# Kernel optimization log

Measured on AMD Instinct MI355X. Metric: run time of the kernel, lower is better.

Reference implementation:

```python
import jax, jax.numpy as jnp
import numpy as np

NEG_INF = -100000000.0  # matches masked_fill value in torch source

def setup_inputs() -> dict:
    key = jax.random.key(0)
    ks = jax.random.split(key, 7)
    d_model, d = 1024, 128
    B, S = 4, 2048
    scale = 1.0 / np.sqrt(d_model)
    x = jax.random.normal(ks[0], (B, S, d_model), dtype=jnp.float32)
    Wq = jax.random.normal(ks[1], (d, d_model), dtype=jnp.float32) * scale
    bq = jax.random.normal(ks[2], (d,), dtype=jnp.float32) * 0.02
    Wk = jax.random.normal(ks[3], (d, d_model), dtype=jnp.float32) * scale
    bk = jax.random.normal(ks[4], (d,), dtype=jnp.float32) * 0.02
    Wv = jax.random.normal(ks[5], (d, d_model), dtype=jnp.float32) * scale
    bv = jax.random.normal(ks[6], (d,), dtype=jnp.float32) * 0.02
    return {"x": x, "Wq": Wq, "bq": bq, "Wk": Wk, "bk": bk, "Wv": Wv, "bv": bv}

def reference(x, Wq, bq, Wk, bk, Wv, bv):
    # Q,K,V: [B,S,d] via torch Linear (x @ W.T + b)
    Q = jnp.einsum('bsm,dm->bsd', x, Wq) + bq
    K = jnp.einsum('bsm,dm->bsd', x, Wk) + bk
    V = jnp.einsum('bsm,dm->bsd', x, Wv) + bv
    d = Wk.shape[0]
    scale = 1.0 / jnp.sqrt(jnp.asarray(d, dtype=Q.dtype))
    scores = jnp.einsum('bqd,bkd->bqk', Q, K) * scale  # [B,S,S]
    # Faithful to source: tril then value-based mask (tril==0 -> -1e8).
    tril = jnp.tril(scores)
    masked = jnp.where(tril == 0, NEG_INF, tril)
    attn = jax.nn.softmax(masked, axis=-1)
    context = jnp.einsum('bqk,bkd->bqd', attn, V)
    return context
```

## Files before the change

### kernel.cpp

```cpp
#include <hip/hip_runtime.h>

typedef __attribute__((ext_vector_type(8))) short bf16x8;
typedef __attribute__((ext_vector_type(4))) float f32x4;

__device__ __forceinline__ unsigned short f2bf(float f) {
    unsigned int u = __float_as_uint(f);
    u += 0x7fffu + ((u >> 16) & 1u);
    return (unsigned short)(u >> 16);
}
__device__ __forceinline__ unsigned int pack2bf(float lo, float hi) {
    return (unsigned int)f2bf(lo) | ((unsigned int)f2bf(hi) << 16);
}
__device__ __forceinline__ void async_ld16(void* lds, const void* g) {
    __builtin_amdgcn_global_load_lds(
        (const __attribute__((address_space(1))) unsigned int*)g,
        (__attribute__((address_space(3))) unsigned int*)lds, 16, 0, 0);
}

__global__ __launch_bounds__(256) void convert_bf16(
    const float* __restrict__ x,
    const float* __restrict__ Wq, const float* __restrict__ Wk,
    const float* __restrict__ Wv,
    unsigned short* __restrict__ xbf, unsigned short* __restrict__ Wcat)
{
    const size_t XN8 = (size_t)8192 * 1024 / 8;
    const size_t TN8 = XN8 + (size_t)3 * 128 * 1024 / 8;
    size_t i = (size_t)blockIdx.x * blockDim.x + threadIdx.x;
    const size_t stride = (size_t)gridDim.x * blockDim.x;
    for (; i < TN8; i += stride) {
        const float* src;
        unsigned short* dst;
        if (i < XN8) {
            src = x + i * 8;
            dst = xbf + i * 8;
        } else {
            size_t o = (i - XN8) * 8;
            int sel = (int)(o >> 17);
            const float* W = (sel == 0) ? Wq : ((sel == 1) ? Wk : Wv);
            src = W + (o & 131071);
            dst = Wcat + o;
        }
        float4 f0 = ((const float4*)src)[0];
        float4 f1 = ((const float4*)src)[1];
        uint4 u;
        u.x = pack2bf(f0.x, f0.y); u.y = pack2bf(f0.z, f0.w);
        u.z = pack2bf(f1.x, f1.y); u.w = pack2bf(f1.z, f1.w);
        *(uint4*)dst = u;
    }
}

__global__ __launch_bounds__(256) void qkv_gemm(
    const unsigned short* __restrict__ xbf,
    const unsigned short* __restrict__ Wcat,
    const float* __restrict__ bq, const float* __restrict__ bk,
    const float* __restrict__ bv,
    unsigned short* __restrict__ Qg,
    unsigned short* __restrict__ Kg,
    unsigned short* __restrict__ Vtg)
{
    __shared__ unsigned short As[64 * 64];
    __shared__ unsigned short Bs[128 * 64];

    const int tid  = threadIdx.x;
    const int lane = tid & 63;
    const int w    = tid >> 6;
    const int quad = lane >> 4;
    const int ln   = lane & 15;
    const int wm   = w >> 1, wn = w & 1;
    const int lr   = lane >> 3;
    const int lc   = (lane & 7) * 8;

    const int bid   = blockIdx.x;
    const int mbase = (bid / 3) * 64;
    const int nb    = bid % 3;
    const unsigned short* Wsel = Wcat + (size_t)nb * 128 * 1024;

    f32x4 acc[2][4];
#pragma unroll
    for (int mt = 0; mt < 2; mt++)
#pragma unroll
        for (int nt = 0; nt < 4; nt++) acc[mt][nt] = (f32x4){0.f, 0.f, 0.f, 0.f};

    for (int kb = 0; kb < 16; kb++) {
        __syncthreads();
        const int kcol = kb * 64 + lc;
#pragma unroll
        for (int j = 0; j < 2; j++) {
            int chunk = w * 2 + j;
            int row = chunk * 8 + lr;
            async_ld16(&As[chunk * 512 + lane * 8],
                       xbf + (size_t)(mbase + row) * 1024 + kcol);
        }
#pragma unroll
        for (int j = 0; j < 4; j++) {
            int chunk = w * 4 + j;
            int row = chunk * 8 + lr;
            async_ld16(&Bs[chunk * 512 + lane * 8],
                       Wsel + (size_t)row * 1024 + kcol);
        }
        __syncthreads();
#pragma unroll
        for (int ks = 0; ks < 2; ks++) {
            bf16x8 a[2], b[4];
#pragma unroll
            for (int mt = 0; mt < 2; mt++)
                a[mt] = *(const bf16x8*)&As[(wm * 32 + mt * 16 + ln) * 64 + ks * 32 + quad * 8];
#pragma unroll
            for (int nt = 0; nt < 4; nt++)
                b[nt] = *(const bf16x8*)&Bs[(wn * 64 + nt * 16 + ln) * 64 + ks * 32 + quad * 8];
#pragma unroll
            for (int mt = 0; mt < 2; mt++)
#pragma unroll
                for (int nt = 0; nt < 4; nt++)
                    acc[mt][nt] = __builtin_amdgcn_mfma_f32_16x16x32_bf16(
                        a[mt], b[nt], acc[mt][nt], 0, 0, 0);
        }
    }

    const float scale = (nb == 0) ? 0.08838834764831845f : 1.0f;
    const float* bsel = (nb == 0) ? bq : ((nb == 1) ? bk : bv);
    float bias_v[4];
#pragma unroll
    for (int nt = 0; nt < 4; nt++) bias_v[nt] = bsel[wn * 64 + nt * 16 + ln];

    if (nb < 2) {
        unsigned short* dst = (nb == 0) ? Qg : Kg;
#pragma unroll
        for (int mt = 0; mt < 2; mt++)
#pragma unroll
            for (int nt = 0; nt < 4; nt++)
#pragma unroll
                for (int r = 0; r < 4; r++) {
                    int m = mbase + wm * 32 + mt * 16 + quad * 4 + r;
                    int d = wn * 64 + nt * 16 + ln;
                    dst[(size_t)m * 128 + d] =
                        f2bf((acc[mt][nt][r] + bias_v[nt]) * scale);
                }
    } else {
#pragma unroll
        for (int mt = 0; mt < 2; mt++)
#pragma unroll
            for (int nt = 0; nt < 4; nt++) {
                int dd = wn * 64 + nt * 16 + ln;
                int m0 = mbase + wm * 32 + mt * 16 + quad * 4;
                int bb = m0 >> 11, s0 = m0 & 2047;
                ushort4 u = { f2bf(acc[mt][nt][0] + bias_v[nt]),
                              f2bf(acc[mt][nt][1] + bias_v[nt]),
                              f2bf(acc[mt][nt][2] + bias_v[nt]),
                              f2bf(acc[mt][nt][3] + bias_v[nt]) };
                *(ushort4*)&Vtg[((size_t)bb * 128 + dd) * 2048 + s0] = u;
            }
    }
}

__global__ __launch_bounds__(256) void flash_attn(
    const unsigned short* __restrict__ Qg,
    const unsigned short* __restrict__ Kg,
    const unsigned short* __restrict__ Vtg,
    unsigned short* __restrict__ Opart,
    float2* __restrict__ ml)
{
    constexpr int LQ = 136, LV = 72, LP = 72;
    __shared__ unsigned short Qs[64][LQ];
    __shared__ unsigned short Ks[64][LQ];
    __shared__ unsigned short Vts[128][LV];
    __shared__ unsigned short Pl[64][LP];

    const int b = blockIdx.x;
    const int q = blockIdx.y;
    const int c = blockIdx.z;
    if (c > (q >> 2)) return;

    const int m4 = q >> 2, r4 = q & 3;
    const int pidx = b * 144 + q + 2 * m4 * (m4 - 1) + r4 * m4 + c;
    const int k0 = c * 4;
    const int kend = (c * 4 + 4 < q + 1) ? (c * 4 + 4) : (q + 1);

    const int q0   = q * 64;
    const int tid  = threadIdx.x;
    const int lane = tid & 63, w = tid >> 6, quad = lane >> 4, ln = lane & 15;

    {
        int col = (tid & 15) * 8;
#pragma unroll
        for (int i = 0; i < 4; i++) {
            int row = (tid >> 4) + i * 16;
            *(uint4*)&Qs[row][col] =
                *(const uint4*)&Qg[((size_t)b * 2048 + q0 + row) * 128 + col];
        }
    }

    float m_i[4], l_i[4];
    f32x4 Ofr[8];
#pragma unroll
    for (int r = 0; r < 4; r++) { m_i[r] = -__builtin_inff(); l_i[r] = 0.f; }
#pragma unroll
    for (int dt = 0; dt < 8; dt++) Ofr[dt] = (f32x4){0.f, 0.f, 0.f, 0.f};

    for (int kt = k0; kt < kend; kt++) {
        __syncthreads();
        {
            int col = (tid & 15) * 8;
#pragma unroll
            for (int i = 0; i < 4; i++) {
                int row = (tid >> 4) + i * 16;
                *(uint4*)&Ks[row][col] =
                    *(const uint4*)&Kg[((size_t)b * 2048 + kt * 64 + row) * 128 + col];
            }
            int c2 = (tid & 7) * 8;
#pragma unroll
            for (int i = 0; i < 4; i++) {
                int dd = (tid >> 3) + i * 32;
                *(uint4*)&Vts[dd][c2] =
                    *(const uint4*)&Vtg[((size_t)b * 128 + dd) * 2048 + kt * 64 + c2];
            }
        }
        __syncthreads();

        bf16x8 qa[4];
#pragma unroll
        for (int ks = 0; ks < 4; ks++)
            qa[ks] = *(const bf16x8*)&Qs[w * 16 + ln][ks * 32 + quad * 8];
        f32x4 sfr[4];
#pragma unroll
        for (int ct = 0; ct < 4; ct++) {
            f32x4 s = (f32x4){0.f, 0.f, 0.f, 0.f};
#pragma unroll
            for (int ks = 0; ks < 4; ks++) {
                bf16x8 kf = *(const bf16x8*)&Ks[ct * 16 + ln][ks * 32 + quad * 8];
                s = __builtin_amdgcn_mfma_f32_16x16x32_bf16(qa[ks], kf, s, 0, 0, 0);
            }
            sfr[ct] = s;
        }

        if (kt == q) {
#pragma unroll
            for (int ct = 0; ct < 4; ct++)
#pragma unroll
                for (int r = 0; r < 4; r++)
                    if (ct * 16 + ln > w * 16 + quad * 4 + r)
                        sfr[ct][r] = -__builtin_inff();
        }

        float mrow[4];
#pragma unroll
        for (int r = 0; r < 4; r++) mrow[r] = -__builtin_inff();
#pragma unroll
        for (int ct = 0; ct < 4; ct++)
#pragma unroll
            for (int r = 0; r < 4; r++) mrow[r] = fmaxf(mrow[r], sfr[ct][r]);
#pragma unroll
        for (int off = 1; off < 16; off <<= 1)
#pragma unroll
            for (int r = 0; r < 4; r++)
                mrow[r] = fmaxf(mrow[r], __shfl_xor(mrow[r], off, 64));

        float alpha[4], rs[4];
#pragma unroll
        for (int r = 0; r < 4; r++) {
            float mn = fmaxf(m_i[r], mrow[r]);
            alpha[r] = __expf(m_i[r] - mn);
            m_i[r]   = mn;
            rs[r]    = 0.f;
        }
#pragma unroll
        for (int ct = 0; ct < 4; ct++)
#pragma unroll
            for (int r = 0; r < 4; r++) {
                float p = __expf(sfr[ct][r] - m_i[r]);
                rs[r] += p;
                Pl[w * 16 + quad * 4 + r][ct * 16 + ln] = f2bf(p);
            }
#pragma unroll
        for (int off = 1; off < 16; off <<= 1)
#pragma unroll
            for (int r = 0; r < 4; r++) rs[r] += __shfl_xor(rs[r], off, 64);
#pragma unroll
        for (int r = 0; r < 4; r++) l_i[r] = l_i[r] * alpha[r] + rs[r];
#pragma unroll
        for (int dt = 0; dt < 8; dt++)
#pragma unroll
            for (int r = 0; r < 4; r++) Ofr[dt][r] *= alpha[r];

        __syncthreads();

#pragma unroll
        for (int kstep = 0; kstep < 2; kstep++) {
            bf16x8 pa = *(const bf16x8*)&Pl[w * 16 + ln][kstep * 32 + quad * 8];
#pragma unroll
            for (int dt = 0; dt < 8; dt++) {
                bf16x8 vf = *(const bf16x8*)&Vts[dt * 16 + ln][kstep * 32 + quad * 8];
                Ofr[dt] = __builtin_amdgcn_mfma_f32_16x16x32_bf16(pa, vf, Ofr[dt], 0, 0, 0);
            }
        }
    }

#pragma unroll
    for (int dt = 0; dt < 8; dt++)
#pragma unroll
        for (int r = 0; r < 4; r++) {
            int row = w * 16 + quad * 4 + r;
            Opart[((size_t)pidx * 64 + row) * 128 + dt * 16 + ln] = f2bf(Ofr[dt][r]);
        }
    if (ln == 0) {
#pragma unroll
        for (int r = 0; r < 4; r++) {
            int row = w * 16 + quad * 4 + r;
            ml[(size_t)pidx * 64 + row] = make_float2(m_i[r], l_i[r]);
        }
    }
}

__global__ __launch_bounds__(256) void combine(
    const unsigned short* __restrict__ Opart,
    const float2* __restrict__ ml,
    float* __restrict__ out)
{
    const int b = blockIdx.x >> 5, q = blockIdx.x & 31;
    const int m4 = q >> 2, r4 = q & 3;
    const int pbase = b * 144 + q + 2 * m4 * (m4 - 1) + r4 * m4;
    const int nc = m4 + 1;

    const int row = threadIdx.x >> 2;
    const int cg  = (threadIdx.x & 3) * 32;

    float mc[8], lc[8], wgt[8];
    float mmax = -__builtin_inff();
    for (int c = 0; c < nc; c++) {
        float2 t = ml[(size_t)(pbase + c) * 64 + row];
        mc[c] = t.x; lc[c] = t.y;
        mmax = fmaxf(mmax, t.x);
    }
    float lsum = 0.f;
    for (int c = 0; c < nc; c++) {
        wgt[c] = __expf(mc[c] - mmax);
        lsum += lc[c] * wgt[c];
    }
    const float inv = 1.0f / lsum;

    for (int v = 0; v < 4; v++) {
        int col = cg + v * 8;
        float acc[8];
#pragma unroll
        for (int k = 0; k < 8; k++) acc[k] = 0.f;
        for (int c = 0; c < nc; c++) {
            uint4 u = *(const uint4*)&Opart[((size_t)(pbase + c) * 64 + row) * 128 + col];
            float f0 = __uint_as_float(u.x << 16);
            float f1 = __uint_as_float(u.x & 0xffff0000u);
            float f2 = __uint_as_float(u.y << 16);
            float f3 = __uint_as_float(u.y & 0xffff0000u);
            float f4 = __uint_as_float(u.z << 16);
            float f5 = __uint_as_float(u.z & 0xffff0000u);
            float f6 = __uint_as_float(u.w << 16);
            float f7 = __uint_as_float(u.w & 0xffff0000u);
            float wc = wgt[c];
            acc[0] += wc * f0; acc[1] += wc * f1; acc[2] += wc * f2; acc[3] += wc * f3;
            acc[4] += wc * f4; acc[5] += wc * f5; acc[6] += wc * f6; acc[7] += wc * f7;
        }
        float* o = &out[((size_t)b * 2048 + q * 64 + row) * 128 + col];
        float4 o0 = { acc[0] * inv, acc[1] * inv, acc[2] * inv, acc[3] * inv };
        float4 o1 = { acc[4] * inv, acc[5] * inv, acc[6] * inv, acc[7] * inv };
        ((float4*)o)[0] = o0;
        ((float4*)o)[1] = o1;
    }
}

extern "C" void kernel_launch(void* const* d_in, const int* in_sizes, int n_in,
                              void* d_out, int out_size, void* d_ws, size_t ws_size,
                              hipStream_t stream) {
    const float* x  = (const float*)d_in[0];
    const float* Wq = (const float*)d_in[1];
    const float* bq = (const float*)d_in[2];
    const float* Wk = (const float*)d_in[3];
    const float* bk = (const float*)d_in[4];
    const float* Wv = (const float*)d_in[5];
    const float* bv = (const float*)d_in[6];
    float* out = (float*)d_out;

    char* wsb = (char*)d_ws;
    unsigned short* xbf  = (unsigned short*)wsb;
    unsigned short* Wcat = (unsigned short*)(wsb + 16777216);
    unsigned short* Opart = (unsigned short*)wsb;
    float2*         ml   = (float2*)(wsb + 9437184);
    unsigned short* Qg   = (unsigned short*)(wsb + 17563648);
    unsigned short* Kg   = Qg + (size_t)8192 * 128;
    unsigned short* Vtg  = Qg + (size_t)2 * 8192 * 128;

    convert_bf16<<<1024, 256, 0, stream>>>(x, Wq, Wk, Wv, xbf, Wcat);
    qkv_gemm<<<384, 256, 0, stream>>>(xbf, Wcat, bq, bk, bv, Qg, Kg, Vtg);
    flash_attn<<<dim3(4, 32, 8), 256, 0, stream>>>(Qg, Kg, Vtg, Opart, ml);
    combine<<<128, 256, 0, stream>>>(Opart, ml, out);
}
```

Measured before the change: 145.2 us.

## Double-buffer async loads in GEMM and attention, retile GEMM, flatten convert grid

The QKV GEMM moves to 32-row tiles with double-buffered LDS and async global-to-LDS loads for the next k-block, and doubles its grid. Flash attention keeps Q fragments in registers and double-buffers K/V tiles through async LDS loads, removing the Qs buffer and the padded layouts. The convert kernel drops its grid-stride loop and uses one thread per 8 elements. The combine kernel fully unrolls over a fixed eight chunks with clamped indices and remaps threads so consecutive threads handle consecutive rows. This aims to overlap memory latency with MFMA work and raise occupancy, but the unpadded K and V LDS layouts may cause bank conflicts, and the unrolled combine issues redundant loads for the clamped chunks.

```diff
diff --git a/kernel.cpp b/kernel.cpp
--- a/kernel.cpp
+++ b/kernel.cpp
@@ -24,29 +24,25 @@
     unsigned short* __restrict__ xbf, unsigned short* __restrict__ Wcat)
 {
     const size_t XN8 = (size_t)8192 * 1024 / 8;
-    const size_t TN8 = XN8 + (size_t)3 * 128 * 1024 / 8;
-    size_t i = (size_t)blockIdx.x * blockDim.x + threadIdx.x;
-    const size_t stride = (size_t)gridDim.x * blockDim.x;
-    for (; i < TN8; i += stride) {
-        const float* src;
-        unsigned short* dst;
-        if (i < XN8) {
-            src = x + i * 8;
-            dst = xbf + i * 8;
-        } else {
-            size_t o = (i - XN8) * 8;
-            int sel = (int)(o >> 17);
-            const float* W = (sel == 0) ? Wq : ((sel == 1) ? Wk : Wv);
-            src = W + (o & 131071);
-            dst = Wcat + o;
-        }
-        float4 f0 = ((const float4*)src)[0];
-        float4 f1 = ((const float4*)src)[1];
-        uint4 u;
-        u.x = pack2bf(f0.x, f0.y); u.y = pack2bf(f0.z, f0.w);
-        u.z = pack2bf(f1.x, f1.y); u.w = pack2bf(f1.z, f1.w);
-        *(uint4*)dst = u;
-    }
+    size_t i = (size_t)blockIdx.x * 256 + threadIdx.x;
+    const float* src;
+    unsigned short* dst;
+    if (i < XN8) {
+        src = x + i * 8;
+        dst = xbf + i * 8;
+    } else {
+        size_t o = (i - XN8) * 8;
+        int sel = (int)(o >> 17);
+        const float* W = (sel == 0) ? Wq : ((sel == 1) ? Wk : Wv);
+        src = W + (o & 131071);
+        dst = Wcat + o;
+    }
+    float4 f0 = ((const float4*)src)[0];
+    float4 f1 = ((const float4*)src)[1];
+    uint4 u;
+    u.x = pack2bf(f0.x, f0.y); u.y = pack2bf(f0.z, f0.w);
+    u.z = pack2bf(f1.x, f1.y); u.w = pack2bf(f1.z, f1.w);
+    *(uint4*)dst = u;
 }
 
 __global__ __launch_bounds__(256) void qkv_gemm(
@@ -58,81 +54,81 @@
     unsigned short* __restrict__ Kg,
     unsigned short* __restrict__ Vtg)
 {
-    __shared__ unsigned short As[64 * 64];
-    __shared__ unsigned short Bs[128 * 64];
+    __shared__ unsigned short As[2][32 * 64];
+    __shared__ unsigned short Bs[2][128 * 64];
 
     const int tid  = threadIdx.x;
     const int lane = tid & 63;
     const int w    = tid >> 6;
     const int quad = lane >> 4;
     const int ln   = lane & 15;
-    const int wm   = w >> 1, wn = w & 1;
     const int lr   = lane >> 3;
     const int lc   = (lane & 7) * 8;
 
     const int bid   = blockIdx.x;
-    const int mbase = (bid / 3) * 64;
+    const int mbase = (bid / 3) * 32;
     const int nb    = bid % 3;
     const unsigned short* Wsel = Wcat + (size_t)nb * 128 * 1024;
-
-    f32x4 acc[2][4];
+    const unsigned short* xrowA = xbf + (size_t)(mbase + w * 8 + lr) * 1024 + lc;
+
+    f32x4 acc[2][2];
 #pragma unroll
     for (int mt = 0; mt < 2; mt++)
 #pragma unroll
-        for (int nt = 0; nt < 4; nt++) acc[mt][nt] = (f32x4){0.f, 0.f, 0.f, 0.f};
-
-    for (int kb = 0; kb < 16; kb++) {
-        __syncthreads();
-        const int kcol = kb * 64 + lc;
-#pragma unroll
-        for (int j = 0; j < 2; j++) {
-            int chunk = w * 2 + j;
-            int row = chunk * 8 + lr;
-            async_ld16(&As[chunk * 512 + lane * 8],
-                       xbf + (size_t)(mbase + row) * 1024 + kcol);
-        }
+        for (int nt = 0; nt < 2; nt++) acc[mt][nt] = (f32x4){0.f, 0.f, 0.f, 0.f};
+
+    auto stage = [&](int kb, int p) {
+        const int kcol = kb * 64;
+        async_ld16(&As[p][w * 512 + lane * 8], xrowA + kcol);
 #pragma unroll
         for (int j = 0; j < 4; j++) {
             int chunk = w * 4 + j;
-            int row = chunk * 8 + lr;
-            async_ld16(&Bs[chunk * 512 + lane * 8],
-                       Wsel + (size_t)row * 1024 + kcol);
-        }
-        __syncthreads();
+            async_ld16(&Bs[p][chunk * 512 + lane * 8],
+                       Wsel + (size_t)(chunk * 8 + lr) * 1024 + kcol + lc);
+        }
+    };
+
+    stage(0, 0);
+    __syncthreads();
+
+    for (int kb = 0; kb < 16; kb++) {
+        const int p = kb & 1;
+        if (kb < 15) stage(kb + 1, p ^ 1);
 #pragma unroll
         for (int ks = 0; ks < 2; ks++) {
-            bf16x8 a[2], b[4];
+            bf16x8 a[2], b[2];
 #pragma unroll
             for (int mt = 0; mt < 2; mt++)
-                a[mt] = *(const bf16x8*)&As[(wm * 32 + mt * 16 + ln) * 64 + ks * 32 + quad * 8];
-#pragma unroll
-            for (int nt = 0; nt < 4; nt++)
-                b[nt] = *(const bf16x8*)&Bs[(wn * 64 + nt * 16 + ln) * 64 + ks * 32 + quad * 8];
+                a[mt] = *(const bf16x8*)&As[p][(mt * 16 + ln) * 64 + ks * 32 + quad * 8];
+#pragma unroll
+            for (int nt = 0; nt < 2; nt++)
+                b[nt] = *(const bf16x8*)&Bs[p][(w * 32 + nt * 16 + ln) * 64 + ks * 32 + quad * 8];
 #pragma unroll
             for (int mt = 0; mt < 2; mt++)
 #pragma unroll
-                for (int nt = 0; nt < 4; nt++)
+                for (int nt = 0; nt < 2; nt++)
                     acc[mt][nt] = __builtin_amdgcn_mfma_f32_16x16x32_bf16(
                         a[mt], b[nt], acc[mt][nt], 0, 0, 0);
         }
+        __syncthreads();
     }
 
     const float scale = (nb == 0) ? 0.08838834764831845f : 1.0f;
     const float* bsel = (nb == 0) ? bq : ((nb == 1) ? bk : bv);
-    float bias_v[4];
-#pragma unroll
-    for (int nt = 0; nt < 4; nt++) bias_v[nt] = bsel[wn * 64 + nt * 16 + ln];
+    float bias_v[2];
+#pragma unroll
+    for (int nt = 0; nt < 2; nt++) bias_v[nt] = bsel[w * 32 + nt * 16 + ln];
 
     if (nb < 2) {
         unsigned short* dst = (nb == 0) ? Qg : Kg;
 #pragma unroll
         for (int mt = 0; mt < 2; mt++)
 #pragma unroll
-            for (int nt = 0; nt < 4; nt++)
+            for (int nt = 0; nt < 2; nt++)
 #pragma unroll
                 for (int r = 0; r < 4; r++) {
-                    int m = mbase + wm * 32 + mt * 16 + quad * 4 + r;
-                    int d = wn * 64 + nt * 16 + ln;
+                    int m = mbase + mt * 16 + quad * 4 + r;
+                    int d = w * 32 + nt * 16 + ln;
                     dst[(size_t)m * 128 + d] =
                         f2bf((acc[mt][nt][r] + bias_v[nt]) * scale);
                 }
@@ -140,9 +136,9 @@
 #pragma unroll
         for (int mt = 0; mt < 2; mt++)
 #pragma unroll
-            for (int nt = 0; nt < 4; nt++) {
-                int dd = wn * 64 + nt * 16 + ln;
-                int m0 = mbase + wm * 32 + mt * 16 + quad * 4;
+            for (int nt = 0; nt < 2; nt++) {
+                int dd = w * 32 + nt * 16 + ln;
+                int m0 = mbase + mt * 16 + quad * 4;
                 int bb = m0 >> 11, s0 = m0 & 2047;
                 ushort4 u = { f2bf(acc[mt][nt][0] + bias_v[nt]),
                               f2bf(acc[mt][nt][1] + bias_v[nt]),
@@ -160,11 +156,9 @@
     unsigned short* __restrict__ Opart,
     float2* __restrict__ ml)
 {
-    constexpr int LQ = 136, LV = 72, LP = 72;
-    __shared__ unsigned short Qs[64][LQ];
-    __shared__ unsigned short Ks[64][LQ];
-    __shared__ unsigned short Vts[128][LV];
-    __shared__ unsigned short Pl[64][LP];
+    __shared__ unsigned short Ks[2][64 * 128];
+    __shared__ unsigned short Vts[2][128 * 64];
+    __shared__ unsigned short Pl[64][72];
 
     const int b = blockIdx.x;
     const int q = blockIdx.y;
@@ -176,19 +170,31 @@
     const int k0 = c * 4;
     const int kend = (c * 4 + 4 < q + 1) ? (c * 4 + 4) : (q + 1);
 
-    const int q0   = q * 64;
     const int tid  = threadIdx.x;
     const int lane = tid & 63, w = tid >> 6, quad = lane >> 4, ln = lane & 15;
 
-    {
-        int col = (tid & 15) * 8;
-#pragma unroll
-        for (int i = 0; i < 4; i++) {
-            int row = (tid >> 4) + i * 16;
-            *(uint4*)&Qs[row][col] =
-                *(const uint4*)&Qg[((size_t)b * 2048 + q0 + row) * 128 + col];
-        }
-    }
+    bf16x8 qa[4];
+    const unsigned short* qrow =
+        Qg + ((size_t)b * 2048 + q * 64 + w * 16 + ln) * 128 + quad * 8;
+#pragma unroll
+    for (int ks = 0; ks < 4; ks++) qa[ks] = *(const bf16x8*)(qrow + ks * 32);
+
+    auto stage = [&](int kt, int p) {
+        const unsigned short* ksrc = Kg + ((size_t)b * 2048 + kt * 64) * 128;
+#pragma unroll
+        for (int j = 0; j < 4; j++) {
+            int chunk = w * 4 + j;
+            async_ld16(&Ks[p][chunk * 512 + lane * 8],
+                       ksrc + (size_t)(chunk * 4 + (lane >> 4)) * 128 + (lane & 15) * 8);
+        }
+        const unsigned short* vsrc = Vtg + (size_t)b * 128 * 2048 + kt * 64;
+#pragma unroll
+        for (int j = 0; j < 4; j++) {
+            int chunk = w * 4 + j;
+            async_ld16(&Vts[p][chunk * 512 + lane * 8],
+                       vsrc + (size_t)(chunk * 8 + (lane >> 3)) * 2048 + (lane & 7) * 8);
+        }
+    };
 
     float m_i[4], l_i[4];
     f32x4 Ofr[8];
@@ -197,37 +203,20 @@
 #pragma unroll
     for (int dt = 0; dt < 8; dt++) Ofr[dt] = (f32x4){0.f, 0.f, 0.f, 0.f};
 
+    stage(k0, 0);
+    __syncthreads();
+
+    int p = 0;
     for (int kt = k0; kt < kend; kt++) {
-        __syncthreads();
-        {
-            int col = (tid & 15) * 8;
-#pragma unroll
-            for (int i = 0; i < 4; i++) {
-                int row = (tid >> 4) + i * 16;
-                *(uint4*)&Ks[row][col] =
-                    *(const uint4*)&Kg[((size_t)b * 2048 + kt * 64 + row) * 128 + col];
-            }
-            int c2 = (tid & 7) * 8;
-#pragma unroll
-            for (int i = 0; i < 4; i++) {
-                int dd = (tid >> 3) + i * 32;
-                *(uint4*)&Vts[dd][c2] =
-                    *(const uint4*)&Vtg[((size_t)b * 128 + dd) * 2048 + kt * 64 + c2];
-            }
-        }
-        __syncthreads();
-
-        bf16x8 qa[4];
-#pragma unroll
-        for (int ks = 0; ks < 4; ks++)
-            qa[ks] = *(const bf16x8*)&Qs[w * 16 + ln][ks * 32 + quad * 8];
+        if (kt + 1 < kend) stage(kt + 1, p ^ 1);
+
         f32x4 sfr[4];
 #pragma unroll
         for (int ct = 0; ct < 4; ct++) {
             f32x4 s = (f32x4){0.f, 0.f, 0.f, 0.f};
 #pragma unroll
             for (int ks = 0; ks < 4; ks++) {
-                bf16x8 kf = *(const bf16x8*)&Ks[ct * 16 + ln][ks * 32 + quad * 8];
+                bf16x8 kf = *(const bf16x8*)&Ks[p][(ct * 16 + ln) * 128 + ks * 32 + quad * 8];
                 s = __builtin_amdgcn_mfma_f32_16x16x32_bf16(qa[ks], kf, s, 0, 0, 0);
             }
             sfr[ct] = s;
@@ -267,9 +256,9 @@
         for (int ct = 0; ct < 4; ct++)
 #pragma unroll
             for (int r = 0; r < 4; r++) {
-                float p = __expf(sfr[ct][r] - m_i[r]);
-                rs[r] += p;
-                Pl[w * 16 + quad * 4 + r][ct * 16 + ln] = f2bf(p);
+                float pv = __expf(sfr[ct][r] - m_i[r]);
+                rs[r] += pv;
+                Pl[w * 16 + quad * 4 + r][ct * 16 + ln] = f2bf(pv);
             }
 #pragma unroll
         for (int off = 1; off < 16; off <<= 1)
@@ -289,10 +278,12 @@
             bf16x8 pa = *(const bf16x8*)&Pl[w * 16 + ln][kstep * 32 + quad * 8];
 #pragma unroll
             for (int dt = 0; dt < 8; dt++) {
-                bf16x8 vf = *(const bf16x8*)&Vts[dt * 16 + ln][kstep * 32 + quad * 8];
+                bf16x8 vf = *(const bf16x8*)&Vts[p][(dt * 16 + ln) * 64 + kstep * 32 + quad * 8];
                 Ofr[dt] = __builtin_amdgcn_mfma_f32_16x16x32_bf16(pa, vf, Ofr[dt], 0, 0, 0);
             }
         }
+        __syncthreads();
+        p ^= 1;
     }
 
 #pragma unroll
@@ -321,41 +312,50 @@
     const int pbase = b * 144 + q + 2 * m4 * (m4 - 1) + r4 * m4;
     const int nc = m4 + 1;
 
-    const int row = threadIdx.x >> 2;
-    const int cg  = (threadIdx.x & 3) * 32;
-
+    const int row = threadIdx.x & 63;
+    const int grp = (threadIdx.x >> 6) * 32;
+
+    float2 t[8];
+#pragma unroll
+    for (int c2 = 0; c2 < 8; c2++) {
+        int cc = (c2 < nc) ? c2 : (nc - 1);
+        t[c2] = ml[(size_t)(pbase + cc) * 64 + row];
+    }
     float mc[8], lc[8], wgt[8];
     float mmax = -__builtin_inff();
-    for (int c = 0; c < nc; c++) {
-        float2 t = ml[(size_t)(pbase + c) * 64 + row];
-        mc[c] = t.x; lc[c] = t.y;
-        mmax = fmaxf(mmax, t.x);
+#pragma unroll
+    for (int c2 = 0; c2 < 8; c2++) {
+        mc[c2] = (c2 < nc) ? t[c2].x : -__builtin_inff();
+        lc[c2] = (c2 < nc) ? t[c2].y : 0.f;
+        mmax = fmaxf(mmax, mc[c2]);
     }
     float lsum = 0.f;
-    for (int c = 0; c < nc; c++) {
-        wgt[c] = __expf(mc[c] - mmax);
-        lsum += lc[c] * wgt[c];
+#pragma unroll
+    for (int c2 = 0; c2 < 8; c2++) {
+        wgt[c2] = __expf(mc[c2] - mmax);
+        lsum += lc[c2] * wgt[c2];
     }
     const float inv = 1.0f / lsum;
 
+#pragma unroll
     for (int v = 0; v < 4; v++) {
-        int col = cg + v * 8;
+        int col = grp + v * 8;
         float acc[8];
 #pragma unroll
         for (int k = 0; k < 8; k++) acc[k] = 0.f;
-        for (int c = 0; c < nc; c++) {
-            uint4 u = *(const uint4*)&Opart[((size_t)(pbase + c) * 64 + row) * 128 + col];
-            float f0 = __uint_as_float(u.x << 16);
-            float f1 = __uint_as_float(u.x & 0xffff0000u);
-            float f2 = __uint_as_float(u.y << 16);
-            float f3 = __uint_as_float(u.y & 0xffff0000u);
-            float f4 = __uint_as_float(u.z << 16);
-            float f5 = __uint_as_float(u.z & 0xffff0000u);
-            float f6 = __uint_as_float(u.w << 16);
-            float f7 = __uint_as_float(u.w & 0xffff0000u);
-            float wc = wgt[c];
-            acc[0] += wc * f0; acc[1] += wc * f1; acc[2] += wc * f2; acc[3] += wc * f3;
-            acc[4] += wc * f4; acc[5] += wc * f5; acc[6] += wc * f6; acc[7] += wc * f7;
+#pragma unroll
+        for (int c2 = 0; c2 < 8; c2++) {
+            int cc = (c2 < nc) ? c2 : (nc - 1);
+            uint4 u = *(const uint4*)&Opart[((size_t)(pbase + cc) * 64 + row) * 128 + col];
+            float wc = wgt[c2];
+            acc[0] += wc * __uint_as_float(u.x << 16);
+            acc[1] += wc * __uint_as_float(u.x & 0xffff0000u);
+            acc[2] += wc * __uint_as_float(u.y << 16);
+            acc[3] += wc * __uint_as_float(u.y & 0xffff0000u);
+            acc[4] += wc * __uint_as_float(u.z << 16);
+            acc[5] += wc * __uint_as_float(u.z & 0xffff0000u);
+            acc[6] += wc * __uint_as_float(u.w << 16);
+            acc[7] += wc * __uint_as_float(u.w & 0xffff0000u);
         }
         float* o = &out[((size_t)b * 2048 + q * 64 + row) * 128 + col];
         float4 o0 = { acc[0] * inv, acc[1] * inv, acc[2] * inv, acc[3] * inv };
@@ -378,16 +378,16 @@
     float* out = (float*)d_out;
 
     char* wsb = (char*)d_ws;
-    unsigned short* xbf  = (unsigned short*)wsb;
-    unsigned short* Wcat = (unsigned short*)(wsb + 16777216);
+    unsigned short* xbf   = (unsigned short*)wsb;
+    unsigned short* Wcat  = (unsigned short*)(wsb + 16777216);
     unsigned short* Opart = (unsigned short*)wsb;
-    float2*         ml   = (float2*)(wsb + 9437184);
-    unsigned short* Qg   = (unsigned short*)(wsb + 17563648);
-    unsigned short* Kg   = Qg + (size_t)8192 * 128;
-    unsigned short* Vtg  = Qg + (size_t)2 * 8192 * 128;
-
-    convert_bf16<<<1024, 256, 0, stream>>>(x, Wq, Wk, Wv, xbf, Wcat);
-    qkv_gemm<<<384, 256, 0, stream>>>(xbf, Wcat, bq, bk, bv, Qg, Kg, Vtg);
+    float2*         ml    = (float2*)(wsb + 9437184);
+    unsigned short* Qg    = (unsigned short*)(wsb + 17563648);
+    unsigned short* Kg    = Qg + (size_t)8192 * 128;
+    unsigned short* Vtg   = Qg + (size_t)2 * 8192 * 128;
+
+    convert_bf16<<<4288, 256, 0, stream>>>(x, Wq, Wk, Wv, xbf, Wcat);
+    qkv_gemm<<<768, 256, 0, stream>>>(xbf, Wcat, bq, bk, bv, Qg, Kg, Vtg);
     flash_attn<<<dim3(4, 32, 8), 256, 0, stream>>>(Qg, Kg, Vtg, Opart, ml);
     combine<<<128, 256, 0, stream>>>(Opart, ml, out);
 }
```

Measured after the change: 155.8 us. +7.4%, slower.
